# Kernel tuning notes

Hardware: AMD Instinct MI355X
Metric: run time of the kernel (lower is better)

Reference implementation:

```python
import jax, jax.numpy as jnp
import numpy as np

N, K, D = 65536, 1024, 512


def setup_inputs() -> dict:
    key = jax.random.key(0)
    k1, k2, k3 = jax.random.split(key, 3)
    x = jax.random.normal(k1, (N, D), dtype=jnp.float32)
    y = jax.random.randint(k2, (N,), 0, K)  # true/assigned cluster labels
    centers = jax.random.normal(k3, (K, D), dtype=jnp.float32)  # nn.Parameter
    return {"x": x, "y": y, "centers": centers}


def reference(x, y, centers):
    # caldis: squared euclidean distance from every point to every center.
    # original expand+sub+square+sum without materializing [N, K, D]).
    x2 = jnp.sum(x * x, axis=1, keepdims=True)          # [N, 1]
    c2 = jnp.sum(centers * centers, axis=1)              # [K]
    distance = x2 - 2.0 * (x @ centers.T) + c2           # [N, K]

    # predict: torch.sort(distance)[1][:, 0] == index of the smallest distance
    ynew = jnp.argmin(distance, axis=1)                  # [N]

    # calwei + calloss: one-hot(y) * distance summed == gather distance[i, y[i]]
    loss = jnp.sum(jnp.take_along_axis(distance, y[:, None], axis=1))

    return loss, ynew
```

## Files before the change

### kernel.cpp

```cpp
#include <hip/hip_runtime.h>

#define NPTS 65536
#define KC   1024
#define DD   512

using bf16x8 = __attribute__((ext_vector_type(8))) __bf16;
using f32x4  = __attribute__((ext_vector_type(4))) float;

__device__ __forceinline__ void gld_lds16(const void* g, void* lds_base) {
  __builtin_amdgcn_global_load_lds(
      (const __attribute__((address_space(1))) unsigned int*)(uintptr_t)g,
      (__attribute__((address_space(3))) unsigned int*)(unsigned int)(uintptr_t)lds_base,
      16, 0, 0);
}

__device__ __forceinline__ uint2 pack4(const float4& v) {
  uint2 r;
  r.x = (__float_as_uint(v.x) >> 16) | (__float_as_uint(v.y) & 0xffff0000u);
  r.y = (__float_as_uint(v.z) >> 16) | (__float_as_uint(v.w) & 0xffff0000u);
  return r;
}


__global__ __launch_bounds__(256) void prep_kernel(
    const float* __restrict__ x, const int* __restrict__ y,
    const float* __restrict__ centers, uint4* __restrict__ xb,
    uint4* __restrict__ cb, float* __restrict__ c2,
    float* __restrict__ partial) {
  const int w = threadIdx.x >> 6, l = threadIdx.x & 63;
  if (blockIdx.x >= 4096) {
    const int row = (blockIdx.x - 4096) * 4 + w;
    const float4* cf4 = (const float4*)centers;
    float4 a = cf4[row * 128 + 2 * l];
    float4 b = cf4[row * 128 + 2 * l + 1];
    uint2 pa = pack4(a), pb = pack4(b);
    cb[row * 64 + l] = make_uint4(pa.x, pa.y, pb.x, pb.y);
    float s = a.x * a.x + a.y * a.y + a.z * a.z + a.w * a.w +
              b.x * b.x + b.y * b.y + b.z * b.z + b.w * b.w;
#pragma unroll
    for (int off = 32; off; off >>= 1) s += __shfl_down(s, off, 64);
    if (l == 0) c2[row] = s;
    return;
  }
  const int rbase = blockIdx.x * 16 + w * 4;
  const float4* xr = (const float4*)(x + (size_t)rbase * DD);
  float4 a[4], b[4];
#pragma unroll
  for (int r = 0; r < 4; r++) {
    a[r] = xr[r * 128 + 2 * l];
    b[r] = xr[r * 128 + 2 * l + 1];
  }
  int yr[4];
#pragma unroll
  for (int r = 0; r < 4; r++) yr[r] = y[rbase + r];
  float4 ca[4], cb4[4];
#pragma unroll
  for (int r = 0; r < 4; r++) {
    const float4* cr = (const float4*)(centers + (size_t)yr[r] * DD);
    ca[r]  = cr[2 * l];
    cb4[r] = cr[2 * l + 1];
  }
#pragma unroll
  for (int r = 0; r < 4; r++) {
    uint2 pa = pack4(a[r]), pb = pack4(b[r]);
    xb[(size_t)(rbase + r) * 64 + l] = make_uint4(pa.x, pa.y, pb.x, pb.y);
  }
  float s = 0.f;
#pragma unroll
  for (int r = 0; r < 4; r++) {
    float d0 = a[r].x - ca[r].x, d1 = a[r].y - ca[r].y;
    float d2 = a[r].z - ca[r].z, d3 = a[r].w - ca[r].w;
    float d4 = b[r].x - cb4[r].x, d5 = b[r].y - cb4[r].y;
    float d6 = b[r].z - cb4[r].z, d7 = b[r].w - cb4[r].w;
    s += d0 * d0 + d1 * d1 + d2 * d2 + d3 * d3 +
         d4 * d4 + d5 * d5 + d6 * d6 + d7 * d7;
  }
#pragma unroll
  for (int off = 32; off; off >>= 1) s += __shfl_down(s, off, 64);
  __shared__ float ps[4];
  if (l == 0) ps[w] = s;
  __syncthreads();
  if (threadIdx.x == 0) partial[blockIdx.x] = ps[0] + ps[1] + ps[2] + ps[3];
}

__global__ __launch_bounds__(512, 2) void gemm_argmin(
    const uint4* __restrict__ xb, const uint4* __restrict__ cb,
    const float* __restrict__ c2, const float* __restrict__ partial,
    float* __restrict__ loss_out, float* __restrict__ ynew_out) {
  __shared__ uint4 As[4096];
  __shared__ uint4 Bs[4096];
  __shared__ float c2s[KC];
  __shared__ float ls[8];

  const int t = threadIdx.x;
  const int w = t >> 6, l = t & 63;
  const int wm = w >> 1, wn = w & 1;
  const int q4 = l >> 4, m16 = l & 15;
  const int row0 = blockIdx.x * 256;

  c2s[t] = c2[t];
  c2s[t + 512] = c2[t + 512];

  const int srow = l >> 2;
  const int schk = (l & 3) ^ ((l >> 3) & 3);
  const uint4* aB = xb + ((size_t)(row0 + w * 16 + srow) * 64 + schk);
  const uint4* bB = cb + ((size_t)(w * 16 + srow) * 64 + schk);
  const int xs = q4 ^ ((m16 >> 1) & 3);

#pragma unroll
  for (int p = 0; p < 3; p++) {
    const int sp = p * 1024;
    const int oa = p * 4;
    gld_lds16(aB + oa, &As[sp + w * 64]);
    gld_lds16(aB + 8192 + oa, &As[sp + w * 64 + 512]);
    gld_lds16(bB + oa, &Bs[sp + w * 64]);
    gld_lds16(bB + 8192 + oa, &Bs[sp + w * 64 + 512]);
  }

  f32x4 acc[4][8];
#pragma unroll
  for (int i = 0; i < 4; i++)
#pragma unroll
    for (int j = 0; j < 8; j++) acc[i][j] = (f32x4){0.f, 0.f, 0.f, 0.f};

  float best[16];
  int bi_[16];
#pragma unroll
  for (int i = 0; i < 16; i++) { best[i] = 3.4e38f; bi_[i] = 0; }

  asm volatile("s_waitcnt vmcnt(4)" ::: "memory");
  __builtin_amdgcn_s_barrier();

  bf16x8 afA[4], afB[4], bfP[4], bfQ[4];
#pragma unroll
  for (int i = 0; i < 4; i++)
    afA[i] = *(const bf16x8*)&As[(wm * 64 + i * 16 + m16) * 4 + xs];
#pragma unroll
  for (int j = 0; j < 4; j++)
    bfP[j] = *(const bf16x8*)&Bs[(wn * 128 + j * 16 + m16) * 4 + xs];

#define FOLD_P(P)                                                           \
  {                                                                         \
    const int n0f = (P) * 256;                                              \
    _Pragma("unroll")                                                       \
    for (int j = 0; j < 8; j++) {                                           \
      const int n = n0f + wn * 128 + j * 16 + m16;                          \
      const float cc = c2s[n];                                              \
      _Pragma("unroll")                                                     \
      for (int i = 0; i < 4; i++)                                           \
        _Pragma("unroll")                                                   \
        for (int r = 0; r < 4; r++) {                                       \
          float v = fmaf(-2.f, acc[i][j][r], cc);                           \
          const int bidx = i * 4 + r;                                       \
          if (v < best[bidx]) { best[bidx] = v; bi_[bidx] = n; }            \
          acc[i][j][r] = 0.f;                                               \
        }                                                                   \
    }                                                                       \
  }

#define TILE_BODY(T, AFC, AFN)                                              \
  {                                                                         \
    const int bse = ((T) & 3) * 1024;                                       \
         \
    if ((T) <= 60) {                                                        \
      const int s2 = (((T) + 3) & 3) * 1024;                                \
      const int oa = (((T) + 3) & 15) * 4;                                  \
      gld_lds16(aB + oa, &As[s2 + w * 64]);                                 \
      gld_lds16(aB + 8192 + oa, &As[s2 + w * 64 + 512]);                    \
    }                                                                       \
    if ((T) < 63) {                                                         \
      const int bn = (((T) + 1) & 3) * 1024;                                \
      _Pragma("unroll")                                                     \
      for (int i = 0; i < 4; i++)                                           \
        AFN[i] = *(const bf16x8*)&As[bn + (wm * 64 + i * 16 + m16) * 4 + xs]; \
    }                                                                       \
    _Pragma("unroll")                                                       \
    for (int j = 0; j < 4; j++)                                             \
      bfQ[j] = *(const bf16x8*)&Bs[bse + (wn * 128 + (j + 4) * 16 + m16) * 4 + xs]; \
    __builtin_amdgcn_s_setprio(1);                                          \
    _Pragma("unroll")                                                       \
    for (int j = 0; j < 4; j++)                                             \
      _Pragma("unroll")                                                     \
      for (int i = 0; i < 4; i++)                                           \
        acc[i][j] = __builtin_amdgcn_mfma_f32_16x16x32_bf16(AFC[i], bfP[j], acc[i][j], 0, 0, 0); \
    __builtin_amdgcn_s_setprio(0);                                          \
                 \
    if ((T) <= 60) {                                                        \
      const int s2 = (((T) + 3) & 3) * 1024;                                \
      const int ob = (((T) + 3) >> 4) * 16384 + (((T) + 3) & 15) * 4;       \
      gld_lds16(bB + ob, &Bs[s2 + w * 64]);                                 \
      gld_lds16(bB + ob + 8192, &Bs[s2 + w * 64 + 512]);                    \
    }                                                                       \
    if ((T) < 63) {                                                         \
      const int bn = (((T) + 1) & 3) * 1024;                                \
      _Pragma("unroll")                                                     \
      for (int j = 0; j < 4; j++)                                           \
        bfP[j] = *(const bf16x8*)&Bs[bn + (wn * 128 + j * 16 + m16) * 4 + xs]; \
    }                                                                       \
    __builtin_amdgcn_s_setprio(1);                                          \
    _Pragma("unroll")                                                       \
    for (int j = 0; j < 4; j++)                                             \
      _Pragma("unroll")                                                     \
      for (int i = 0; i < 4; i++)                                           \
        acc[i][j + 4] = __builtin_amdgcn_mfma_f32_16x16x32_bf16(AFC[i], bfQ[j], acc[i][j + 4], 0, 0, 0); \
    __builtin_amdgcn_s_setprio(0);                                          \
    if (((T) & 15) == 15) FOLD_P((T) >> 4);                                 \
    if ((T) <= 60)      asm volatile("s_waitcnt vmcnt(4)" ::: "memory");    \
    else if ((T) < 63)  asm volatile("s_waitcnt vmcnt(0)" ::: "memory");    \
    __builtin_amdgcn_s_barrier();                                           \
  }

#pragma unroll 1
  for (int s = 0; s < 32; ++s) {
    const int te = 2 * s;
    TILE_BODY(te, afA, afB);
    TILE_BODY(te + 1, afB, afA);
  }
#undef TILE_BODY
#undef FOLD_P

  float* mv = (float*)As;
  int*   mi = (int*)((char*)As + 2048);
#pragma unroll
  for (int bi = 0; bi < 16; bi++) {
    float v = best[bi];
    int idx = bi_[bi];
#pragma unroll
    for (int off = 8; off; off >>= 1) {
      float ov = __shfl_xor(v, off, 64);
      int oi = __shfl_xor(idx, off, 64);
      if (ov < v || (ov == v && oi < idx)) { v = ov; idx = oi; }
    }
    if (m16 == 0) {
      const int m = wm * 64 + (bi >> 2) * 16 + q4 * 4 + (bi & 3);
      mv[wn * 256 + m] = v;
      mi[wn * 256 + m] = idx;
    }
  }
  __syncthreads();
  if (t < 256) {
    float v0 = mv[t], v1 = mv[256 + t];
    int i0 = mi[t], i1 = mi[256 + t];
    const int idx = (v1 < v0 || (v1 == v0 && i1 < i0)) ? i1 : i0;
    ynew_out[row0 + t] = (float)idx;
  }

  if (blockIdx.x == 0) {
    float s = 0.f;
#pragma unroll
    for (int j = 0; j < 8; j++) s += partial[t + 512 * j];
#pragma unroll
    for (int off = 32; off; off >>= 1) s += __shfl_down(s, off, 64);
    if (l == 0) ls[w] = s;
    __syncthreads();
    if (t == 0) {
      float tot = 0.f;
#pragma unroll
      for (int i = 0; i < 8; i++) tot += ls[i];
      loss_out[0] = tot;
    }
  }
}

__global__ __launch_bounds__(256) void loss_final(const float* __restrict__ partial,
                                                  float* __restrict__ out) {
  float s = 0.f;
#pragma unroll
  for (int j = 0; j < 64; j++) s += partial[threadIdx.x + 256 * j];
#pragma unroll
  for (int off = 32; off; off >>= 1) s += __shfl_down(s, off, 64);
  __shared__ float ps[4];
  if ((threadIdx.x & 63) == 0) ps[threadIdx.x >> 6] = s;
  __syncthreads();
  if (threadIdx.x == 0) out[0] = ps[0] + ps[1] + ps[2] + ps[3];
}


#define SLOT(row, oct) (16 * (oct) + (((row) & 15) ^ (((oct) & 2) << 1)))

__device__ __forceinline__ void split_pack(const float4& a, const float4& b,
                                           uint4& hi, uint4& lo) {
  float f[8] = {a.x, a.y, a.z, a.w, b.x, b.y, b.z, b.w};
  uint hw[4], lw[4];
#pragma unroll
  for (int i = 0; i < 4; i++) {
    uint e0 = __float_as_uint(f[2 * i]), e1 = __float_as_uint(f[2 * i + 1]);
    hw[i] = (e0 >> 16) | (e1 & 0xffff0000u);
    float l0 = f[2 * i]     - __uint_as_float(e0 & 0xffff0000u);
    float l1 = f[2 * i + 1] - __uint_as_float(e1 & 0xffff0000u);
    lw[i] = (__float_as_uint(l0) >> 16) | (__float_as_uint(l1) & 0xffff0000u);
  }
  hi = make_uint4(hw[0], hw[1], hw[2], hw[3]);
  lo = make_uint4(lw[0], lw[1], lw[2], lw[3]);
}

__global__ __launch_bounds__(256) void c2_kernel(const float* __restrict__ centers,
                                                 float* __restrict__ c2) {
  int wave = (blockIdx.x * 256 + threadIdx.x) >> 6;
  int lane = threadIdx.x & 63;
  const float4* c4 = (const float4*)(centers + (size_t)wave * DD);
  float s = 0.f;
#pragma unroll
  for (int j = 0; j < 2; j++) {
    float4 v = c4[lane + 64 * j];
    s += v.x * v.x + v.y * v.y + v.z * v.z + v.w * v.w;
  }
#pragma unroll
  for (int off = 32; off; off >>= 1) s += __shfl_down(s, off, 64);
  if (lane == 0) c2[wave] = s;
}

__global__ __launch_bounds__(256, 2) void argmin_fb(
    const float* __restrict__ x, const float* __restrict__ centers,
    const float* __restrict__ c2, float* __restrict__ ynew_out) {
  __shared__ uint4 Ah[512], Al[512], Bh[512], Bl[512];
  const int t = threadIdx.x;
  const int w = t >> 6, l = t & 63;
  const int wm = w >> 1, wn = w & 1;
  const size_t row0 = (size_t)blockIdx.x * 128;
  const int srow = t >> 1, h = t & 1;
  const int mt = srow >> 4;
  const int so0 = mt * 64 + SLOT(srow, 2 * h);
  const int so1 = mt * 64 + SLOT(srow, 2 * h + 1);
  const int rs = SLOT(l & 15, l >> 4);
  const float* xp = x + (row0 + srow) * DD + h * 16;
  float best[16];
  int bidx[16];
#pragma unroll
  for (int i = 0; i < 16; i++) { best[i] = 3.4e38f; bidx[i] = 0; }
  for (int n0 = 0; n0 < KC; n0 += 128) {
    const float* bp = centers + (size_t)(n0 + srow) * DD + h * 16;
    f32x4 acc[4][4];
#pragma unroll
    for (int i = 0; i < 4; i++)
#pragma unroll
      for (int j = 0; j < 4; j++) acc[i][j] = (f32x4){0.f, 0.f, 0.f, 0.f};
    float4 ra[4], rb[4];
#pragma unroll
    for (int q = 0; q < 4; q++) {
      ra[q] = *(const float4*)(xp + q * 4);
      rb[q] = *(const float4*)(bp + q * 4);
    }
    for (int ks = 0; ks < 16; ks++) {
      uint4 ah0, al0, ah1, al1, bh0, bl0, bh1, bl1;
      split_pack(ra[0], ra[1], ah0, al0);
      split_pack(ra[2], ra[3], ah1, al1);
      split_pack(rb[0], rb[1], bh0, bl0);
      split_pack(rb[2], rb[3], bh1, bl1);
      __syncthreads();
      Ah[so0] = ah0; Al[so0] = al0;
      Ah[so1] = ah1; Al[so1] = al1;
      Bh[so0] = bh0; Bl[so0] = bl0;
      Bh[so1] = bh1; Bl[so1] = bl1;
      __syncthreads();
      if (ks < 15) {
#pragma unroll
        for (int q = 0; q < 4; q++) {
          ra[q] = *(const float4*)(xp + (ks + 1) * 32 + q * 4);
          rb[q] = *(const float4*)(bp + (ks + 1) * 32 + q * 4);
        }
      }
      bf16x8 afh[4], afl[4], bfh[4], bfl[4];
#pragma unroll
      for (int i = 0; i < 4; i++) {
        afh[i] = *(const bf16x8*)&Ah[(wm * 4 + i) * 64 + rs];
        afl[i] = *(const bf16x8*)&Al[(wm * 4 + i) * 64 + rs];
        bfh[i] = *(const bf16x8*)&Bh[(wn * 4 + i) * 64 + rs];
        bfl[i] = *(const bf16x8*)&Bl[(wn * 4 + i) * 64 + rs];
      }
#pragma unroll
      for (int i = 0; i < 4; i++)
#pragma unroll
        for (int j = 0; j < 4; j++) {
          acc[i][j] = __builtin_amdgcn_mfma_f32_16x16x32_bf16(afh[i], bfh[j], acc[i][j], 0, 0, 0);
          acc[i][j] = __builtin_amdgcn_mfma_f32_16x16x32_bf16(afl[i], bfh[j], acc[i][j], 0, 0, 0);
          acc[i][j] = __builtin_amdgcn_mfma_f32_16x16x32_bf16(afh[i], bfl[j], acc[i][j], 0, 0, 0);
        }
    }
#pragma unroll
    for (int j = 0; j < 4; j++) {
      int n = n0 + wn * 64 + j * 16 + (l & 15);
      float cc = c2[n];
#pragma unroll
      for (int i = 0; i < 4; i++)
#pragma unroll
        for (int r = 0; r < 4; r++) {
          float v = fmaf(-2.f, acc[i][j][r], cc);
          int bi = i * 4 + r;
          if (v < best[bi]) { best[bi] = v; bidx[bi] = n; }
        }
    }
  }
#pragma unroll
  for (int bi = 0; bi < 16; bi++) {
    float v = best[bi];
    int idx = bidx[bi];
#pragma unroll
    for (int off = 8; off; off >>= 1) {
      float ov = __shfl_xor(v, off, 64);
      int oi = __shfl_xor(idx, off, 64);
      if (ov < v || (ov == v && oi < idx)) { v = ov; idx = oi; }
    }
    if ((l & 15) == 0) {
      int m = wm * 64 + (bi >> 2) * 16 + (l >> 4) * 4 + (bi & 3);
      ynew_out[row0 + m] = (float)idx;
    }
  }
}

__global__ __launch_bounds__(256) void loss_partial_fb(
    const float* __restrict__ x, const int* __restrict__ y,
    const float* __restrict__ centers, float* __restrict__ partial) {
  const int w = threadIdx.x >> 6, l = threadIdx.x & 63;
  const int row = blockIdx.x * 4 + w;
  const float4* x4 = (const float4*)(x + (size_t)row * DD);
  const float4* c4 = (const float4*)(centers + (size_t)y[row] * DD);
  float s = 0.f;
#pragma unroll
  for (int j = 0; j < 2; j++) {
    float4 xv = x4[2 * l + j], cv = c4[2 * l + j];
    float dx = xv.x - cv.x, dy = xv.y - cv.y, dz = xv.z - cv.z, dw = xv.w - cv.w;
    s += dx * dx + dy * dy + dz * dz + dw * dw;
  }
#pragma unroll
  for (int off = 32; off; off >>= 1) s += __shfl_down(s, off, 64);
  __shared__ float ps[4];
  if (l == 0) ps[w] = s;
  __syncthreads();
  if (threadIdx.x == 0) partial[blockIdx.x] = ps[0] + ps[1] + ps[2] + ps[3];
}


extern "C" void kernel_launch(void* const* d_in, const int* in_sizes, int n_in,
                              void* d_out, int out_size, void* d_ws, size_t ws_size,
                              hipStream_t stream) {
  const float* x       = (const float*)d_in[0];
  const int*   y       = (const int*)d_in[1];
  const float* centers = (const float*)d_in[2];
  float* out = (float*)d_out;

  const size_t xb_bytes = (size_t)NPTS * DD * 2;
  const size_t cb_bytes = (size_t)KC * DD * 2;
  const size_t need = xb_bytes + cb_bytes + (KC + NPTS / 4) * sizeof(float);

  if (ws_size >= need) {
    uint4* xb      = (uint4*)d_ws;
    uint4* cbp     = (uint4*)((char*)d_ws + xb_bytes);
    float* c2      = (float*)((char*)d_ws + xb_bytes + cb_bytes);
    float* partial = c2 + KC;
    prep_kernel<<<4096 + 256, 256, 0, stream>>>(x, y, centers, xb, cbp, c2, partial);
    gemm_argmin<<<NPTS / 256, 512, 0, stream>>>(xb, cbp, c2, partial, out, out + 1);
  } else {
    float* c2      = (float*)d_ws;
    float* partial = c2 + KC;
    c2_kernel<<<KC / 4, 256, 0, stream>>>(centers, c2);
    argmin_fb<<<NPTS / 128, 256, 0, stream>>>(x, centers, c2, out + 1);
    loss_partial_fb<<<NPTS / 4, 256, 0, stream>>>(x, y, centers, partial);
    loss_final<<<1, 256, 0, stream>>>(partial, out);
  }
}
```

Baseline: 274.7 us.

## Keep full x row-tile resident in LDS and stream centers from global

The GEMM block now covers 128 points and keeps the whole bf16 x tile (all of K=512) in LDS, loaded once during the first 16 k-steps. Center fragments are read straight from a pre-transposed global layout (cbT) into registers, which removes the B-side LDS staging and the per-tile barriers after the first pass. The point is to cut LDS traffic and synchronisation. The cost is that every block re-reads all centers from global/L2 memory, with twice as many blocks and a smaller accumulator tile per wave.

Result: slower. 296.3 us (+7.9%).

```diff
diff --git a/kernel.cpp b/kernel.cpp
--- a/kernel.cpp
+++ b/kernel.cpp
@@ -25,7 +25,7 @@
 __global__ __launch_bounds__(256) void prep_kernel(
     const float* __restrict__ x, const int* __restrict__ y,
     const float* __restrict__ centers, uint4* __restrict__ xb,
-    uint4* __restrict__ cb, float* __restrict__ c2,
+    uint4* __restrict__ cbT, float* __restrict__ c2,
     float* __restrict__ partial) {
   const int w = threadIdx.x >> 6, l = threadIdx.x & 63;
   if (blockIdx.x >= 4096) {
@@ -34,7 +34,7 @@
     float4 a = cf4[row * 128 + 2 * l];
     float4 b = cf4[row * 128 + 2 * l + 1];
     uint2 pa = pack4(a), pb = pack4(b);
-    cb[row * 64 + l] = make_uint4(pa.x, pa.y, pb.x, pb.y);
+    cbT[(l >> 2) * 4096 + row * 4 + (l & 3)] = make_uint4(pa.x, pa.y, pb.x, pb.y);
     float s = a.x * a.x + a.y * a.y + a.z * a.z + a.w * a.w +
               b.x * b.x + b.y * b.y + b.z * b.z + b.w * b.w;
 #pragma unroll
@@ -84,19 +84,18 @@
 }
 
 __global__ __launch_bounds__(512, 2) void gemm_argmin(
-    const uint4* __restrict__ xb, const uint4* __restrict__ cb,
+    const uint4* __restrict__ xb, const uint4* __restrict__ cbT,
     const float* __restrict__ c2, const float* __restrict__ partial,
     float* __restrict__ loss_out, float* __restrict__ ynew_out) {
-  __shared__ uint4 As[4096];
-  __shared__ uint4 Bs[4096];
+  __shared__ uint4 As[8192];
   __shared__ float c2s[KC];
   __shared__ float ls[8];
 
   const int t = threadIdx.x;
   const int w = t >> 6, l = t & 63;
-  const int wm = w >> 1, wn = w & 1;
+  const int wm = w >> 2, wn = w & 3;
   const int q4 = l >> 4, m16 = l & 15;
-  const int row0 = blockIdx.x * 256;
+  const int row0 = blockIdx.x * 128;
 
   c2s[t] = c2[t];
   c2s[t + 512] = c2[t + 512];
@@ -104,47 +103,39 @@
   const int srow = l >> 2;
   const int schk = (l & 3) ^ ((l >> 3) & 3);
   const uint4* aB = xb + ((size_t)(row0 + w * 16 + srow) * 64 + schk);
-  const uint4* bB = cb + ((size_t)(w * 16 + srow) * 64 + schk);
   const int xs = q4 ^ ((m16 >> 1) & 3);
-
-#pragma unroll
-  for (int p = 0; p < 3; p++) {
-    const int sp = p * 1024;
-    const int oa = p * 4;
-    gld_lds16(aB + oa, &As[sp + w * 64]);
-    gld_lds16(aB + 8192 + oa, &As[sp + w * 64 + 512]);
-    gld_lds16(bB + oa, &Bs[sp + w * 64]);
-    gld_lds16(bB + 8192 + oa, &Bs[sp + w * 64 + 512]);
-  }
-
-  f32x4 acc[4][8];
+  const int al0 = (wm * 64 + m16) * 4 + xs;
+  const int bl0 = (wn * 64 + m16) * 4 + q4;
+
+#pragma unroll
+  for (int p = 0; p < 4; p++)
+    gld_lds16(aB + p * 4, &As[p * 512 + w * 64]);
+
+  bf16x8 bA[4], bB[4];
+#pragma unroll
+  for (int j = 0; j < 4; j++)
+    bA[j] = *(const bf16x8*)(cbT + bl0 + j * 64);
+
+  f32x4 acc[4][4];
 #pragma unroll
   for (int i = 0; i < 4; i++)
 #pragma unroll
-    for (int j = 0; j < 8; j++) acc[i][j] = (f32x4){0.f, 0.f, 0.f, 0.f};
+    for (int j = 0; j < 4; j++) acc[i][j] = (f32x4){0.f, 0.f, 0.f, 0.f};
 
   float best[16];
   int bi_[16];
 #pragma unroll
   for (int i = 0; i < 16; i++) { best[i] = 3.4e38f; bi_[i] = 0; }
 
-  asm volatile("s_waitcnt vmcnt(4)" ::: "memory");
+  asm volatile("s_waitcnt vmcnt(7)" ::: "memory");
   __builtin_amdgcn_s_barrier();
 
-  bf16x8 afA[4], afB[4], bfP[4], bfQ[4];
-#pragma unroll
-  for (int i = 0; i < 4; i++)
-    afA[i] = *(const bf16x8*)&As[(wm * 64 + i * 16 + m16) * 4 + xs];
-#pragma unroll
-  for (int j = 0; j < 4; j++)
-    bfP[j] = *(const bf16x8*)&Bs[(wn * 128 + j * 16 + m16) * 4 + xs];
-
-#define FOLD_P(P)                                                           \
+#define FOLD(P)                                                             \
   {                                                                         \
     const int n0f = (P) * 256;                                              \
     _Pragma("unroll")                                                       \
-    for (int j = 0; j < 8; j++) {                                           \
-      const int n = n0f + wn * 128 + j * 16 + m16;                          \
+    for (int j = 0; j < 4; j++) {                                           \
+      const int n = n0f + wn * 64 + j * 16 + m16;                           \
       const float cc = c2s[n];                                              \
       _Pragma("unroll")                                                     \
       for (int i = 0; i < 4; i++)                                           \
@@ -158,66 +149,72 @@
     }                                                                       \
   }
 
-#define TILE_BODY(T, AFC, AFN)                                              \
+#define TILE_P0(T, BC, BN)                                                  \
   {                                                                         \
-    const int bse = ((T) & 3) * 1024;                                       \
-         \
-    if ((T) <= 60) {                                                        \
-      const int s2 = (((T) + 3) & 3) * 1024;                                \
-      const int oa = (((T) + 3) & 15) * 4;                                  \
-      gld_lds16(aB + oa, &As[s2 + w * 64]);                                 \
-      gld_lds16(aB + 8192 + oa, &As[s2 + w * 64 + 512]);                    \
+    const int kt = (T) & 15;                                                \
+    if ((T) < 15) {                                                         \
+      const uint4* bp = cbT + ((T) + 1) * 4096;                             \
+      _Pragma("unroll")                                                     \
+      for (int j = 0; j < 4; j++)                                           \
+        BN[j] = *(const bf16x8*)(bp + bl0 + j * 64);                        \
     }                                                                       \
-    if ((T) < 63) {                                                         \
-      const int bn = (((T) + 1) & 3) * 1024;                                \
-      _Pragma("unroll")                                                     \
-      for (int i = 0; i < 4; i++)                                           \
-        AFN[i] = *(const bf16x8*)&As[bn + (wm * 64 + i * 16 + m16) * 4 + xs]; \
-    }                                                                       \
+    if ((T) < 12)                                                           \
+      gld_lds16(aB + ((T) + 4) * 4, &As[((T) + 4) * 512 + w * 64]);         \
+    bf16x8 af[4];                                                           \
     _Pragma("unroll")                                                       \
-    for (int j = 0; j < 4; j++)                                             \
-      bfQ[j] = *(const bf16x8*)&Bs[bse + (wn * 128 + (j + 4) * 16 + m16) * 4 + xs]; \
-    __builtin_amdgcn_s_setprio(1);                                          \
+    for (int i = 0; i < 4; i++)                                             \
+      af[i] = *(const bf16x8*)&As[kt * 512 + al0 + i * 64];                 \
     _Pragma("unroll")                                                       \
     for (int j = 0; j < 4; j++)                                             \
       _Pragma("unroll")                                                     \
       for (int i = 0; i < 4; i++)                                           \
-        acc[i][j] = __builtin_amdgcn_mfma_f32_16x16x32_bf16(AFC[i], bfP[j], acc[i][j], 0, 0, 0); \
-    __builtin_amdgcn_s_setprio(0);                                          \
-                 \
-    if ((T) <= 60) {                                                        \
-      const int s2 = (((T) + 3) & 3) * 1024;                                \
-      const int ob = (((T) + 3) >> 4) * 16384 + (((T) + 3) & 15) * 4;       \
-      gld_lds16(bB + ob, &Bs[s2 + w * 64]);                                 \
-      gld_lds16(bB + ob + 8192, &Bs[s2 + w * 64 + 512]);                    \
-    }                                                                       \
+        acc[i][j] = __builtin_amdgcn_mfma_f32_16x16x32_bf16(af[i], BC[j], acc[i][j], 0, 0, 0); \
+    if ((T) == 15) FOLD(0);                                                 \
+    if ((T) < 12) asm volatile("s_waitcnt vmcnt(1)" ::: "memory");          \
+    else          asm volatile("s_waitcnt vmcnt(0)" ::: "memory");          \
+    __builtin_amdgcn_s_barrier();                                           \
+  }
+
+#pragma unroll 1
+  for (int s = 0; s < 8; ++s) {
+    const int te = 2 * s;
+    TILE_P0(te, bA, bB);
+    TILE_P0(te + 1, bB, bA);
+  }
+#undef TILE_P0
+
+#define TILE_MAIN(T, BC, BN)                                                \
+  {                                                                         \
+    const int kt = (T) & 15;                                                \
     if ((T) < 63) {                                                         \
-      const int bn = (((T) + 1) & 3) * 1024;                                \
+      const int tn = (T) + 1;                                               \
+      const uint4* bp = cbT + (tn & 15) * 4096 + ((tn >> 4) * 256) * 4;     \
       _Pragma("unroll")                                                     \
       for (int j = 0; j < 4; j++)                                           \
-        bfP[j] = *(const bf16x8*)&Bs[bn + (wn * 128 + j * 16 + m16) * 4 + xs]; \
+        BN[j] = *(const bf16x8*)(bp + bl0 + j * 64);                        \
     }                                                                       \
-    __builtin_amdgcn_s_setprio(1);                                          \
+    bf16x8 af[4];                                                           \
+    _Pragma("unroll")                                                       \
+    for (int i = 0; i < 4; i++)                                             \
+      af[i] = *(const bf16x8*)&As[kt * 512 + al0 + i * 64];                 \
     _Pragma("unroll")                                                       \
     for (int j = 0; j < 4; j++)                                             \
       _Pragma("unroll")                                                     \
       for (int i = 0; i < 4; i++)                                           \
-        acc[i][j + 4] = __builtin_amdgcn_mfma_f32_16x16x32_bf16(AFC[i], bfQ[j], acc[i][j + 4], 0, 0, 0); \
-    __builtin_amdgcn_s_setprio(0);                                          \
-    if (((T) & 15) == 15) FOLD_P((T) >> 4);                                 \
-    if ((T) <= 60)      asm volatile("s_waitcnt vmcnt(4)" ::: "memory");    \
-    else if ((T) < 63)  asm volatile("s_waitcnt vmcnt(0)" ::: "memory");    \
-    __builtin_amdgcn_s_barrier();                                           \
+        acc[i][j] = __builtin_amdgcn_mfma_f32_16x16x32_bf16(af[i], BC[j], acc[i][j], 0, 0, 0); \
+    if (((T) & 15) == 15) FOLD((T) >> 4);                                   \
   }
 
 #pragma unroll 1
-  for (int s = 0; s < 32; ++s) {
+  for (int s = 8; s < 32; ++s) {
     const int te = 2 * s;
-    TILE_BODY(te, afA, afB);
-    TILE_BODY(te + 1, afB, afA);
-  }
-#undef TILE_BODY
-#undef FOLD_P
+    TILE_MAIN(te, bA, bB);
+    TILE_MAIN(te + 1, bB, bA);
+  }
+#undef TILE_MAIN
+#undef FOLD
+
+  __syncthreads();
 
   float* mv = (float*)As;
   int*   mi = (int*)((char*)As + 2048);
@@ -233,15 +230,20 @@
     }
     if (m16 == 0) {
       const int m = wm * 64 + (bi >> 2) * 16 + q4 * 4 + (bi & 3);
-      mv[wn * 256 + m] = v;
-      mi[wn * 256 + m] = idx;
+      mv[wn * 128 + m] = v;
+      mi[wn * 128 + m] = idx;
     }
   }
   __syncthreads();
-  if (t < 256) {
-    float v0 = mv[t], v1 = mv[256 + t];
-    int i0 = mi[t], i1 = mi[256 + t];
-    const int idx = (v1 < v0 || (v1 == v0 && i1 < i0)) ? i1 : i0;
+  if (t < 128) {
+    float v = mv[t];
+    int idx = mi[t];
+#pragma unroll
+    for (int p = 1; p < 4; p++) {
+      float ov = mv[p * 128 + t];
+      int oi = mi[p * 128 + t];
+      if (ov < v || (ov == v && oi < idx)) { v = ov; idx = oi; }
+    }
     ynew_out[row0 + t] = (float)idx;
   }
 
@@ -445,11 +447,11 @@
 
   if (ws_size >= need) {
     uint4* xb      = (uint4*)d_ws;
-    uint4* cbp     = (uint4*)((char*)d_ws + xb_bytes);
+    uint4* cbT     = (uint4*)((char*)d_ws + xb_bytes);
     float* c2      = (float*)((char*)d_ws + xb_bytes + cb_bytes);
     float* partial = c2 + KC;
-    prep_kernel<<<4096 + 256, 256, 0, stream>>>(x, y, centers, xb, cbp, c2, partial);
-    gemm_argmin<<<NPTS / 256, 512, 0, stream>>>(xb, cbp, c2, partial, out, out + 1);
+    prep_kernel<<<4096 + 256, 256, 0, stream>>>(x, y, centers, xb, cbT, c2, partial);
+    gemm_argmin<<<NPTS / 128, 512, 0, stream>>>(xb, cbT, c2, partial, out, out + 1);
   } else {
     float* c2      = (float*)d_ws;
     float* partial = c2 + KC;
```
